# Kernel optimization log

Hardware: AMD Instinct MI355X
Metric: run time of the kernel (lower is better)

Reference implementation:

```python
import jax, jax.numpy as jnp
import numpy as np

G = 8      # groups
H = 64     # hidden size per group
I = 64     # input size per group


def setup_inputs() -> dict:
    key = jax.random.key(0)
    ks = jax.random.split(key, 6)
    B, T = 32, 1000
    s = 1.0 / np.sqrt(H)  # torch GRU init: U(-1/sqrt(hidden), 1/sqrt(hidden))
    x = jax.random.normal(ks[0], (B, T, G * I), dtype=jnp.float32)
    h0 = jnp.zeros((G, B, H), dtype=jnp.float32)
    Wih = jax.random.uniform(ks[1], (G, 3 * H, I), jnp.float32, -s, s)
    Whh = jax.random.uniform(ks[2], (G, 3 * H, H), jnp.float32, -s, s)
    bih = jax.random.uniform(ks[3], (G, 3 * H), jnp.float32, -s, s)
    bhh = jax.random.uniform(ks[4], (G, 3 * H), jnp.float32, -s, s)
    return {"x": x, "h0": h0, "Wih": Wih, "Whh": Whh, "bih": bih, "bhh": bhh}


def reference(x, h0, Wih, Whh, bih, bhh):
    """Grouped GRU: G independent GRUs over last-dim slices of x.
    x: [B,T,G*I], h0: [G,B,H] (detached in original => treated as constant init).
    Returns (output [B,T,G*H], h [G,B,H]) matching torch cat semantics."""
    B, T, _ = x.shape
    xg = x.reshape(B, T, G, I)
    # Precompute input projections for all timesteps: [B,T,G,3H]
    xp = jnp.einsum('btgi,gji->btgj', xg, Wih) + bih
    xp = jnp.moveaxis(xp, 1, 0)  # [T,B,G,3H] for scan
    h_init = jnp.swapaxes(h0, 0, 1)  # [B,G,H]

    def step(h, xpt):
        # h: [B,G,H], xpt: [B,G,3H]
        gh = jnp.einsum('bgh,gjh->bgj', h, Whh) + bhh  # [B,G,3H]
        r = jax.nn.sigmoid(xpt[..., :H] + gh[..., :H])
        z = jax.nn.sigmoid(xpt[..., H:2 * H] + gh[..., H:2 * H])
        n = jnp.tanh(xpt[..., 2 * H:] + r * gh[..., 2 * H:])
        h_new = (1.0 - z) * n + z * h
        return h_new, h_new

    hT, ys = jax.lax.scan(step, h_init, xp)  # ys: [T,B,G,H]
    output = jnp.moveaxis(ys, 0, 1).reshape(B, T, G * H)
    h_final = jnp.swapaxes(hT, 0, 1)  # [G,B,H]
    return output, h_final
```

## Files before the change

kernel.cpp:

```cpp
#include <hip/hip_runtime.h>


#define TPB 256

__device__ __forceinline__ float fast_rcp(float v) { return __builtin_amdgcn_rcpf(v); }
__device__ __forceinline__ float sigm(float v)     { return fast_rcp(1.f + __expf(-v)); }
__device__ __forceinline__ float tanh_f(float v)   { return 1.f - 2.f * fast_rcp(1.f + __expf(2.f * v)); }

__device__ __forceinline__ float4 fma4(float4 a, float4 b, float4 c) {
    c.x = __builtin_fmaf(a.x, b.x, c.x);
    c.y = __builtin_fmaf(a.y, b.y, c.y);
    c.z = __builtin_fmaf(a.z, b.z, c.z);
    c.w = __builtin_fmaf(a.w, b.w, c.w);
    return c;
}

__device__ __forceinline__ float qsum4(float v) {
    int a = __builtin_amdgcn_mov_dpp(__float_as_int(v), 0xB1, 0xF, 0xF, true);
    v += __int_as_float(a);
    int b = __builtin_amdgcn_mov_dpp(__float_as_int(v), 0x4E, 0xF, 0xF, true);
    v += __int_as_float(b);
    return v;
}

__global__ __launch_bounds__(TPB, 1)
void gru_fused(const float* __restrict__ x, const float* __restrict__ h0,
               const float* __restrict__ Wih, const float* __restrict__ Whh,
               const float* __restrict__ bih, const float* __restrict__ bhh,
               float* __restrict__ out, float* __restrict__ hout,
               int B, int T)
{
    const int bid = blockIdx.x;
    const int g   = bid & 7;
    const int b   = bid >> 3;
    const int tid = threadIdx.x;
    const int j   = tid >> 2;
    const int p   = tid & 3;

    const int e0  = tid * 2;
    const int phx = e0 >> 6;
    const int ix  = e0 & 63;

    __shared__ float xsc[2][512];
    __shared__ float hs[2][64];

    const size_t gw = (size_t)g * 192 * 64;
    const float* WhG = Whh + gw;
    const float* WiG = Wih + gw;
    float4 whr[4], whz[4], whn[4], wxr[4], wxz[4], wxn[4];
#pragma unroll
    for (int i = 0; i < 4; ++i) {
        const int col = p * 16 + i * 4;
        whr[i] = *(const float4*)(WhG + (j      ) * 64 + col);
        whz[i] = *(const float4*)(WhG + (j +  64) * 64 + col);
        whn[i] = *(const float4*)(WhG + (j + 128) * 64 + col);
        wxr[i] = *(const float4*)(WiG + (j      ) * 64 + col);
        wxz[i] = *(const float4*)(WiG + (j +  64) * 64 + col);
        wxn[i] = *(const float4*)(WiG + (j + 128) * 64 + col);
    }
    const float* bihG = bih + g * 192;
    const float* bhhG = bhh + g * 192;
    const float b_r  = bihG[j]      + bhhG[j];
    const float b_z  = bihG[64 + j] + bhhG[64 + j];
    const float bi_n = bihG[128 + j];
    const float bh_n = bhhG[128 + j];

    float h_reg = h0[((size_t)g * B + b) * 64 + j];
    if (p == 0) hs[0][j] = h_reg;

    const float* xb = x + (size_t)b * T * 512 + (size_t)g * 64;

    float2 cnext = make_float2(0.f, 0.f);
    {
        float2 c0 = make_float2(0.f, 0.f);
        if (phx < T) c0 = *(const float2*)(xb + (size_t)phx * 512 + ix);
        *(float2*)&xsc[0][e0] = c0;
    }
    asm volatile("s_waitcnt lgkmcnt(0)" ::: "memory");
    __builtin_amdgcn_s_barrier();
    asm volatile("" ::: "memory");

    float* outp = out + (size_t)b * T * 512 + (size_t)g * 64 + j;

    for (int t8 = 0; t8 < T; t8 += 8) {
        const int bufi = (t8 >> 3) & 1;
        const float* xcb = &xsc[bufi][0];
#pragma unroll
        for (int ph = 0; ph < 8; ++ph) {
            const int t = t8 + ph;
            if (t >= T) break;

            if (ph == 0 && t8 + 8 < T)
                cnext = *(const float2*)(xb + (size_t)(t8 + 8 + phx) * 512 + ix);

            const float* hp = &hs[ph & 1][p * 16];
            const float* xp = xcb + ph * 64 + p * 16;

            float4 ar  = make_float4(0.f, 0.f, 0.f, 0.f);
            float4 az  = make_float4(0.f, 0.f, 0.f, 0.f);
            float4 axn = make_float4(0.f, 0.f, 0.f, 0.f);
            float4 ahn = make_float4(0.f, 0.f, 0.f, 0.f);
#pragma unroll
            for (int i = 0; i < 4; ++i) {
                const float4 hv = *(const float4*)(hp + i * 4);
                const float4 xv = *(const float4*)(xp + i * 4);
                ar  = fma4(whr[i], hv, ar);
                az  = fma4(whz[i], hv, az);
                ahn = fma4(whn[i], hv, ahn);
                ar  = fma4(wxr[i], xv, ar);
                az  = fma4(wxz[i], xv, az);
                axn = fma4(wxn[i], xv, axn);
            }
            float sr  = (ar.x  + ar.y ) + (ar.z  + ar.w );
            float sz  = (az.x  + az.y ) + (az.z  + az.w );
            float sxn = (axn.x + axn.y) + (axn.z + axn.w);
            float shn = (ahn.x + ahn.y) + (ahn.z + ahn.w);
            sr = qsum4(sr); sz = qsum4(sz); sxn = qsum4(sxn); shn = qsum4(shn);

            const float r  = sigm(sr + b_r);
            const float zg = sigm(sz + b_z);
            const float nv = tanh_f(sxn + bi_n + r * (shn + bh_n));
            h_reg = nv + zg * (h_reg - nv);

            if (p == 0) hs[(ph & 1) ^ 1][j] = h_reg;
            if (p == 1) outp[(size_t)t * 512] = h_reg;

            if (ph == 7 && t8 + 8 < T)
                *(float2*)&xsc[bufi ^ 1][e0] = cnext;

            asm volatile("s_waitcnt lgkmcnt(0)" ::: "memory");
            __builtin_amdgcn_s_barrier();
            asm volatile("" ::: "memory");
        }
    }

    if (p == 0) hout[((size_t)g * B + b) * 64 + j] = h_reg;
}

extern "C" void kernel_launch(void* const* d_in, const int* in_sizes, int n_in,
                              void* d_out, int out_size, void* d_ws, size_t ws_size,
                              hipStream_t stream) {
    (void)n_in; (void)d_ws; (void)ws_size; (void)out_size;
    const float* x   = (const float*)d_in[0];
    const float* h0  = (const float*)d_in[1];
    const float* Wih = (const float*)d_in[2];
    const float* Whh = (const float*)d_in[3];
    const float* bih = (const float*)d_in[4];
    const float* bhh = (const float*)d_in[5];

    const int B = in_sizes[1] / 512;
    const int T = (int)((long long)in_sizes[0] / ((long long)B * 512));

    float* out  = (float*)d_out;
    float* hout = out + (size_t)B * T * 512;

    dim3 grid(B * 8), block(TPB);
    hipLaunchKernelGGL(gru_fused, grid, block, 0, stream,
                       x, h0, Wih, Whh, bih, bhh, out, hout, B, T);
}
```

Measured before the change: 508.1 us.

## Pack two independent GRU chains per 512-thread block and pin weights in registers

```diff
diff --git a/kernel.cpp b/kernel.cpp
--- a/kernel.cpp
+++ b/kernel.cpp
@@ -1,7 +1,8 @@
 #include <hip/hip_runtime.h>
 
 
-#define TPB 256
+#define TPB 512
+#define CPB 2
 
 __device__ __forceinline__ float fast_rcp(float v) { return __builtin_amdgcn_rcpf(v); }
 __device__ __forceinline__ float sigm(float v)     { return fast_rcp(1.f + __expf(-v)); }
@@ -23,26 +24,30 @@
     return v;
 }
 
-__global__ __launch_bounds__(TPB, 1)
+#define PIN4(v) asm volatile("" : "+v"((v).x), "+v"((v).y), "+v"((v).z), "+v"((v).w))
+
+__global__ __launch_bounds__(TPB)
 void gru_fused(const float* __restrict__ x, const float* __restrict__ h0,
                const float* __restrict__ Wih, const float* __restrict__ Whh,
                const float* __restrict__ bih, const float* __restrict__ bhh,
                float* __restrict__ out, float* __restrict__ hout,
                int B, int T)
 {
-    const int bid = blockIdx.x;
+    const int tid = threadIdx.x;
+    const int cl  = tid >> 8;
+    const int ct  = tid & 255;
+    const int bid = blockIdx.x * CPB + cl;
     const int g   = bid & 7;
     const int b   = bid >> 3;
-    const int tid = threadIdx.x;
-    const int j   = tid >> 2;
-    const int p   = tid & 3;
+    const int j   = ct >> 2;
+    const int p   = ct & 3;
 
-    const int e0  = tid * 2;
+    const int e0  = ct * 2;
     const int phx = e0 >> 6;
     const int ix  = e0 & 63;
 
-    __shared__ float xsc[2][512];
-    __shared__ float hs[2][64];
+    __shared__ float xsc[CPB][2][512];
+    __shared__ float hs[CPB][2][64];
 
     const size_t gw = (size_t)g * 192 * 64;
     const float* WhG = Whh + gw;
@@ -58,15 +63,22 @@
         wxz[i] = *(const float4*)(WiG + (j +  64) * 64 + col);
         wxn[i] = *(const float4*)(WiG + (j + 128) * 64 + col);
     }
+#pragma unroll
+    for (int i = 0; i < 4; ++i) {
+        PIN4(whr[i]); PIN4(whz[i]); PIN4(whn[i]);
+        PIN4(wxr[i]); PIN4(wxz[i]); PIN4(wxn[i]);
+    }
+
     const float* bihG = bih + g * 192;
     const float* bhhG = bhh + g * 192;
-    const float b_r  = bihG[j]      + bhhG[j];
-    const float b_z  = bihG[64 + j] + bhhG[64 + j];
-    const float bi_n = bihG[128 + j];
-    const float bh_n = bhhG[128 + j];
+    float b_r  = bihG[j]      + bhhG[j];
+    float b_z  = bihG[64 + j] + bhhG[64 + j];
+    float bi_n = bihG[128 + j];
+    float bh_n = bhhG[128 + j];
+    asm volatile("" : "+v"(b_r), "+v"(b_z), "+v"(bi_n), "+v"(bh_n));
 
     float h_reg = h0[((size_t)g * B + b) * 64 + j];
-    if (p == 0) hs[0][j] = h_reg;
+    if (p == 0) hs[cl][0][j] = h_reg;
 
     const float* xb = x + (size_t)b * T * 512 + (size_t)g * 64;
 
@@ -74,7 +86,7 @@
     {
         float2 c0 = make_float2(0.f, 0.f);
         if (phx < T) c0 = *(const float2*)(xb + (size_t)phx * 512 + ix);
-        *(float2*)&xsc[0][e0] = c0;
+        *(float2*)&xsc[cl][0][e0] = c0;
     }
     asm volatile("s_waitcnt lgkmcnt(0)" ::: "memory");
     __builtin_amdgcn_s_barrier();
@@ -84,7 +96,7 @@
 
     for (int t8 = 0; t8 < T; t8 += 8) {
         const int bufi = (t8 >> 3) & 1;
-        const float* xcb = &xsc[bufi][0];
+        const float* xcb = &xsc[cl][bufi][0];
 #pragma unroll
         for (int ph = 0; ph < 8; ++ph) {
             const int t = t8 + ph;
@@ -93,7 +105,7 @@
             if (ph == 0 && t8 + 8 < T)
                 cnext = *(const float2*)(xb + (size_t)(t8 + 8 + phx) * 512 + ix);
 
-            const float* hp = &hs[ph & 1][p * 16];
+            const float* hp = &hs[cl][ph & 1][p * 16];
             const float* xp = xcb + ph * 64 + p * 16;
 
             float4 ar  = make_float4(0.f, 0.f, 0.f, 0.f);
@@ -122,11 +134,11 @@
             const float nv = tanh_f(sxn + bi_n + r * (shn + bh_n));
             h_reg = nv + zg * (h_reg - nv);
 
-            if (p == 0) hs[(ph & 1) ^ 1][j] = h_reg;
+            if (p == 0) hs[cl][(ph & 1) ^ 1][j] = h_reg;
             if (p == 1) outp[(size_t)t * 512] = h_reg;
 
             if (ph == 7 && t8 + 8 < T)
-                *(float2*)&xsc[bufi ^ 1][e0] = cnext;
+                *(float2*)&xsc[cl][bufi ^ 1][e0] = cnext;
 
             asm volatile("s_waitcnt lgkmcnt(0)" ::: "memory");
             __builtin_amdgcn_s_barrier();
@@ -154,7 +166,7 @@
     float* out  = (float*)d_out;
     float* hout = out + (size_t)B * T * 512;
 
-    dim3 grid(B * 8), block(TPB);
+    dim3 grid((B * 8) / CPB), block(TPB);
     hipLaunchKernelGGL(gru_fused, grid, block, 0, stream,
                        x, h0, Wih, Whh, bih, bhh, out, hout, B, T);
 }
```

Measured after the change: 649.6 us. 27.8% more time.

## Split each hidden unit's dot products across 8 lanes with 512-thread blocks

Applied to the files above, without the earlier changes.

```diff
diff --git a/kernel.cpp b/kernel.cpp
--- a/kernel.cpp
+++ b/kernel.cpp
@@ -1,12 +1,16 @@
 #include <hip/hip_runtime.h>
 
 
-#define TPB 256
+#define TPB 512
+#define CH  16
 
 __device__ __forceinline__ float fast_rcp(float v) { return __builtin_amdgcn_rcpf(v); }
 __device__ __forceinline__ float sigm(float v)     { return fast_rcp(1.f + __expf(-v)); }
 __device__ __forceinline__ float tanh_f(float v)   { return 1.f - 2.f * fast_rcp(1.f + __expf(2.f * v)); }
 
+__device__ __forceinline__ float4 mul4(float4 a, float4 b) {
+    return make_float4(a.x * b.x, a.y * b.y, a.z * b.z, a.w * b.w);
+}
 __device__ __forceinline__ float4 fma4(float4 a, float4 b, float4 c) {
     c.x = __builtin_fmaf(a.x, b.x, c.x);
     c.y = __builtin_fmaf(a.y, b.y, c.y);
@@ -14,56 +18,69 @@
     c.w = __builtin_fmaf(a.w, b.w, c.w);
     return c;
 }
+__device__ __forceinline__ float hadd4(float4 a) { return (a.x + a.y) + (a.z + a.w); }
 
-__device__ __forceinline__ float qsum4(float v) {
+__device__ __forceinline__ float psum8(float v) {
     int a = __builtin_amdgcn_mov_dpp(__float_as_int(v), 0xB1, 0xF, 0xF, true);
     v += __int_as_float(a);
-    int b = __builtin_amdgcn_mov_dpp(__float_as_int(v), 0x4E, 0xF, 0xF, true);
-    v += __int_as_float(b);
+    a = __builtin_amdgcn_mov_dpp(__float_as_int(v), 0x4E, 0xF, 0xF, true);
+    v += __int_as_float(a);
+    a = __builtin_amdgcn_ds_swizzle(__float_as_int(v), 0x101F);
+    v += __int_as_float(a);
     return v;
 }
 
-__global__ __launch_bounds__(TPB, 1)
+#define PIN4(v) asm volatile("" : "+v"((v).x), "+v"((v).y), "+v"((v).z), "+v"((v).w))
+
+__global__ __launch_bounds__(TPB)
+__attribute__((amdgpu_waves_per_eu(2, 2)))
 void gru_fused(const float* __restrict__ x, const float* __restrict__ h0,
                const float* __restrict__ Wih, const float* __restrict__ Whh,
                const float* __restrict__ bih, const float* __restrict__ bhh,
                float* __restrict__ out, float* __restrict__ hout,
                int B, int T)
 {
+    const int tid = threadIdx.x;
     const int bid = blockIdx.x;
     const int g   = bid & 7;
     const int b   = bid >> 3;
-    const int tid = threadIdx.x;
-    const int j   = tid >> 2;
-    const int p   = tid & 3;
+    const int j   = tid >> 3;
+    const int p   = tid & 7;
 
     const int e0  = tid * 2;
     const int phx = e0 >> 6;
     const int ix  = e0 & 63;
 
-    __shared__ float xsc[2][512];
+    __shared__ float xsc[2][CH * 64];
     __shared__ float hs[2][64];
 
     const size_t gw = (size_t)g * 192 * 64;
     const float* WhG = Whh + gw;
     const float* WiG = Wih + gw;
-    float4 whr[4], whz[4], whn[4], wxr[4], wxz[4], wxn[4];
-#pragma unroll
-    for (int i = 0; i < 4; ++i) {
-        const int col = p * 16 + i * 4;
-        whr[i] = *(const float4*)(WhG + (j      ) * 64 + col);
-        whz[i] = *(const float4*)(WhG + (j +  64) * 64 + col);
-        whn[i] = *(const float4*)(WhG + (j + 128) * 64 + col);
-        wxr[i] = *(const float4*)(WiG + (j      ) * 64 + col);
-        wxz[i] = *(const float4*)(WiG + (j +  64) * 64 + col);
-        wxn[i] = *(const float4*)(WiG + (j + 128) * 64 + col);
-    }
+    const int col = p * 8;
+    float4 whr0, whr1, whz0, whz1, whn0, whn1, wxr0, wxr1, wxz0, wxz1, wxn0, wxn1;
+    whr0 = *(const float4*)(WhG + (j      ) * 64 + col);
+    whr1 = *(const float4*)(WhG + (j      ) * 64 + col + 4);
+    whz0 = *(const float4*)(WhG + (j +  64) * 64 + col);
+    whz1 = *(const float4*)(WhG + (j +  64) * 64 + col + 4);
+    whn0 = *(const float4*)(WhG + (j + 128) * 64 + col);
+    whn1 = *(const float4*)(WhG + (j + 128) * 64 + col + 4);
+    wxr0 = *(const float4*)(WiG + (j      ) * 64 + col);
+    wxr1 = *(const float4*)(WiG + (j      ) * 64 + col + 4);
+    wxz0 = *(const float4*)(WiG + (j +  64) * 64 + col);
+    wxz1 = *(const float4*)(WiG + (j +  64) * 64 + col + 4);
+    wxn0 = *(const float4*)(WiG + (j + 128) * 64 + col);
+    wxn1 = *(const float4*)(WiG + (j + 128) * 64 + col + 4);
+    PIN4(whr0); PIN4(whr1); PIN4(whz0); PIN4(whz1); PIN4(whn0); PIN4(whn1);
+    PIN4(wxr0); PIN4(wxr1); PIN4(wxz0); PIN4(wxz1); PIN4(wxn0); PIN4(wxn1);
+
     const float* bihG = bih + g * 192;
     const float* bhhG = bhh + g * 192;
-    const float b_r  = bihG[j]      + bhhG[j];
-    const float b_z  = bihG[64 + j] + bhhG[64 + j];
-    const float bi_n = bihG[128 + j];
-    const float bh_n = bhhG[128 + j];
+    float b_r  = bihG[j]      + bhhG[j];
+    float b_z  = bihG[64 + j] + bhhG[64 + j];
+    float bi_n = bihG[128 + j];
+    float bh_n = bhhG[128 + j];
+    asm volatile("" : "+v"(b_r), "+v"(b_z), "+v"(bi_n), "+v"(bh_n));
 
     float h_reg = h0[((size_t)g * B + b) * 64 + j];
     if (p == 0) hs[0][j] = h_reg;
@@ -82,40 +99,39 @@
 
     float* outp = out + (size_t)b * T * 512 + (size_t)g * 64 + j;
 
-    for (int t8 = 0; t8 < T; t8 += 8) {
-        const int bufi = (t8 >> 3) & 1;
+    for (int t16 = 0; t16 < T; t16 += CH) {
+        const int bufi = (t16 / CH) & 1;
         const float* xcb = &xsc[bufi][0];
 #pragma unroll
-        for (int ph = 0; ph < 8; ++ph) {
-            const int t = t8 + ph;
+        for (int ph = 0; ph < CH; ++ph) {
+            const int t = t16 + ph;
             if (t >= T) break;
 
-            if (ph == 0 && t8 + 8 < T)
-                cnext = *(const float2*)(xb + (size_t)(t8 + 8 + phx) * 512 + ix);
+            if (ph == 0 && t16 + CH < T) {
+                const int tt = t16 + CH + phx;
+                cnext = (tt < T) ? *(const float2*)(xb + (size_t)tt * 512 + ix)
+                                 : make_float2(0.f, 0.f);
+            }
 
-            const float* hp = &hs[ph & 1][p * 16];
-            const float* xp = xcb + ph * 64 + p * 16;
+            const float* hp = &hs[ph & 1][col];
+            const float* xp = xcb + ph * 64 + col;
 
-            float4 ar  = make_float4(0.f, 0.f, 0.f, 0.f);
-            float4 az  = make_float4(0.f, 0.f, 0.f, 0.f);
-            float4 axn = make_float4(0.f, 0.f, 0.f, 0.f);
-            float4 ahn = make_float4(0.f, 0.f, 0.f, 0.f);
-#pragma unroll
-            for (int i = 0; i < 4; ++i) {
-                const float4 hv = *(const float4*)(hp + i * 4);
-                const float4 xv = *(const float4*)(xp + i * 4);
-                ar  = fma4(whr[i], hv, ar);
-                az  = fma4(whz[i], hv, az);
-                ahn = fma4(whn[i], hv, ahn);
-                ar  = fma4(wxr[i], xv, ar);
-                az  = fma4(wxz[i], xv, az);
-                axn = fma4(wxn[i], xv, axn);
-            }
-            float sr  = (ar.x  + ar.y ) + (ar.z  + ar.w );
-            float sz  = (az.x  + az.y ) + (az.z  + az.w );
-            float sxn = (axn.x + axn.y) + (axn.z + axn.w);
-            float shn = (ahn.x + ahn.y) + (ahn.z + ahn.w);
-            sr = qsum4(sr); sz = qsum4(sz); sxn = qsum4(sxn); shn = qsum4(shn);
+            const float4 h0v = *(const float4*)(hp);
+            const float4 h1v = *(const float4*)(hp + 4);
+            const float4 x0v = *(const float4*)(xp);
+            const float4 x1v = *(const float4*)(xp + 4);
+
+            float4 ar  = mul4(whr0, h0v);  ar  = fma4(whr1, h1v, ar);
+            ar  = fma4(wxr0, x0v, ar);     ar  = fma4(wxr1, x1v, ar);
+            float4 az  = mul4(whz0, h0v);  az  = fma4(whz1, h1v, az);
+            az  = fma4(wxz0, x0v, az);     az  = fma4(wxz1, x1v, az);
+            float4 ahn = mul4(whn0, h0v);  ahn = fma4(whn1, h1v, ahn);
+            float4 axn = mul4(wxn0, x0v);  axn = fma4(wxn1, x1v, axn);
+
+            float sr  = psum8(hadd4(ar));
+            float sz  = psum8(hadd4(az));
+            float sxn = psum8(hadd4(axn));
+            float shn = psum8(hadd4(ahn));
 
             const float r  = sigm(sr + b_r);
             const float zg = sigm(sz + b_z);
@@ -125,7 +141,7 @@
             if (p == 0) hs[(ph & 1) ^ 1][j] = h_reg;
             if (p == 1) outp[(size_t)t * 512] = h_reg;
 
-            if (ph == 7 && t8 + 8 < T)
+            if (ph == CH - 2 && t16 + CH < T)
                 *(float2*)&xsc[bufi ^ 1][e0] = cnext;
 
             asm volatile("s_waitcnt lgkmcnt(0)" ::: "memory");
```

Result: slower. 587.2 us (+15.6%).
